# Kernel optimization log

Measured on AMD Instinct MI355X. Metric: run time of the kernel, lower is better.

Reference implementation:

```python
import jax, jax.numpy as jnp
import numpy as np

NUM_HEADS = 8


def setup_inputs() -> dict:
    key = jax.random.key(0)
    k1, k2 = jax.random.split(key)
    B, N, C = 2, 8192, 512
    x = jax.random.normal(k1, (B, N, C), dtype=jnp.float32)
    # torch nn.Linear weight layout: [out_features, in_features]
    W_qkv = jax.random.normal(k2, (3 * C, C), dtype=jnp.float32) * (C ** -0.5)
    return {"x": x, "W_qkv": W_qkv}


def reference(x, W_qkv):
    B, N, C = x.shape
    H = NUM_HEADS
    d = C // H
    scale = d ** -0.5

    # qkv projection (no bias): [B, N, 3C]
    qkv = x @ W_qkv.T
    # [B, N, 3, H, d] -> [3, B, H, N, d]
    qkv = qkv.reshape(B, N, 3, H, d).transpose(2, 0, 3, 1, 4)
    q, k, v = qkv[0], qkv[1], qkv[2]

    # mean-center keys over sequence dim
    k_hat = k - jnp.mean(k, axis=2, keepdims=True)          # [B, H, N, d]

    # KV aggregation: g = k_hat^T @ v  -> [B, H, d, d]
    g = jnp.einsum('bhnd,bhne->bhde', k_hat, v)

    # k_sum over sequence (numerically ~0 since k_hat is centered, kept faithful)
    k_sum = jnp.sum(k_hat, axis=2)                          # [B, H, d]
    q_ksum = jnp.einsum('bhnd,bhd->bhn', q, k_sum)[..., None]  # [B, H, N, 1]

    # denominator: N*scale + q @ k_sum^T
    t_D = N * scale + q_ksum                                # [B, H, N, 1]
    # numerator: scale + q @ g (broadcast of ones*scale over last dim)
    T_N = scale + jnp.einsum('bhnd,bhde->bhne', q, g)       # [B, H, N, d]

    z = T_N / t_D                                           # [B, H, N, d]
    return z
```

## Files before the change

### kernel.cpp

```cpp
#include <hip/hip_runtime.h>

typedef unsigned short u16;
typedef unsigned int u32;
typedef __attribute__((ext_vector_type(8))) short short8;
typedef __attribute__((ext_vector_type(4))) float f32x4;
typedef __attribute__((ext_vector_type(4))) unsigned short ushort4v;
typedef __attribute__((ext_vector_type(4))) float float4v;

__device__ __forceinline__ float bf2f(u16 u) {
    return __uint_as_float(((u32)u) << 16);
}
__device__ __forceinline__ u16 f2bf(float f) {
    u32 u = __float_as_uint(f);
    u += 0x7FFF + ((u >> 16) & 1);
    return (u16)(u >> 16);
}
__device__ __forceinline__ short8 cvt8(float4 a, float4 b) {
    short8 r;
    r[0] = (short)f2bf(a.x); r[1] = (short)f2bf(a.y);
    r[2] = (short)f2bf(a.z); r[3] = (short)f2bf(a.w);
    r[4] = (short)f2bf(b.x); r[5] = (short)f2bf(b.y);
    r[6] = (short)f2bf(b.z); r[7] = (short)f2bf(b.w);
    return r;
}
__device__ __forceinline__ void stage16(const u16* g, u16* l) {
    __builtin_amdgcn_global_load_lds(
        (const __attribute__((address_space(1))) unsigned int*)g,
        (__attribute__((address_space(3))) unsigned int*)l, 16, 0, 0);
}

__global__ __launch_bounds__(256) void cvt_t(const float* __restrict__ x,
                                             u16* __restrict__ xT,
                                             u16* __restrict__ xb,
                                             float* __restrict__ sp2,
                                             const float* __restrict__ W,
                                             u16* __restrict__ wvb,
                                             u16* __restrict__ Ub) {
    __shared__ __align__(16) char smem[36864];
    const int bid = blockIdx.x;
    const int t = threadIdx.x;
    if (bid >= 1280) {
        const int u = bid - 1280;
        const int h = u >> 4, mt = (u >> 2) & 3, ntt = u & 3;
        u16 (*At)[72] = (u16(*)[72])smem;
        u16 (*Bt)[72] = (u16(*)[72])(smem + 18432);
        const int d = t >> 2, cg = (t & 3) * 32;
        const float* wq = W + (size_t)(h * 64 + d) * 512 + mt * 128 + cg;
        const float* wk = W + (size_t)(512 + h * 64 + d) * 512 + ntt * 128 + cg;
#pragma unroll
        for (int j = 0; j < 32; j += 4) {
            float4 a = *(const float4*)(wq + j);
            float4 kk = *(const float4*)(wk + j);
            At[cg + j + 0][d] = f2bf(a.x); At[cg + j + 1][d] = f2bf(a.y);
            At[cg + j + 2][d] = f2bf(a.z); At[cg + j + 3][d] = f2bf(a.w);
            Bt[cg + j + 0][d] = f2bf(kk.x); Bt[cg + j + 1][d] = f2bf(kk.y);
            Bt[cg + j + 2][d] = f2bf(kk.z); Bt[cg + j + 3][d] = f2bf(kk.w);
        }
        __syncthreads();
        const int l = t & 63, wv = t >> 6;
        const int lr = l & 15, lk = (l >> 4) * 8;
        const int wm = (wv >> 1) * 64, wn = (wv & 1) * 64;
        f32x4 zz = {0.f, 0.f, 0.f, 0.f};
        f32x4 acc[4][4];
        for (int i = 0; i < 4; ++i)
            for (int j = 0; j < 4; ++j) acc[i][j] = zz;
#pragma unroll
        for (int k0 = 0; k0 < 64; k0 += 32) {
            short8 af[4], bfr[4];
#pragma unroll
            for (int mi = 0; mi < 4; ++mi)
                af[mi] = *(const short8*)(&At[wm + mi * 16 + lr][k0 + lk]);
#pragma unroll
            for (int ni = 0; ni < 4; ++ni)
                bfr[ni] = *(const short8*)(&Bt[wn + ni * 16 + lr][k0 + lk]);
#pragma unroll
            for (int mi = 0; mi < 4; ++mi)
#pragma unroll
                for (int ni = 0; ni < 4; ++ni)
                    acc[mi][ni] = __builtin_amdgcn_mfma_f32_16x16x32_bf16(
                        af[mi], bfr[ni], acc[mi][ni], 0, 0, 0);
        }
#pragma unroll
        for (int mi = 0; mi < 4; ++mi)
#pragma unroll
            for (int ni = 0; ni < 4; ++ni) {
                int col = ntt * 128 + wn + ni * 16 + lr;
#pragma unroll
                for (int j = 0; j < 4; ++j) {
                    int row = mt * 128 + wm + mi * 16 + (l >> 4) * 4 + j;
                    Ub[((size_t)(h * 512 + row)) * 512 + col] = f2bf(acc[mi][ni][j]);
                }
            }
        return;
    }
    if (bid >= 1024) {
        const int i = (bid - 1024) * 256 + t;
        float4v v = ((const float4v*)(W + 524288))[i];
        ushort4v r;
        r[0] = f2bf(v[0]); r[1] = f2bf(v[1]); r[2] = f2bf(v[2]); r[3] = f2bf(v[3]);
        ((ushort4v*)wvb)[i] = r;
        return;
    }
    u16 (*tile)[136] = (u16(*)[136])smem;
    const int ct = bid & 3, nt = (bid >> 2) & 127, b = bid >> 9;
    const int r = t >> 2, c0 = (t & 3) * 32;
    const float* src = x + ((size_t)(b * 8192 + nt * 64 + r)) * 512 + ct * 128 + c0;
    short8 r8[4];
#pragma unroll
    for (int j = 0; j < 8; j += 2) {
        float4 v0 = *(const float4*)(src + j * 4);
        float4 v1 = *(const float4*)(src + j * 4 + 4);
        r8[j >> 1] = cvt8(v0, v1);
        *(short8*)(&tile[r][c0 + j * 4]) = r8[j >> 1];
    }
    u16* xbrow = xb + ((size_t)(b * 8192 + nt * 64 + r)) * 512 + ct * 128 + c0;
#pragma unroll
    for (int jj = 0; jj < 4; ++jj) *(short8*)(xbrow + jj * 8) = r8[jj];
    __syncthreads();
    const int c = t >> 1, half = t & 1;
    u16 vals[32];
    float psum = 0.f;
#pragma unroll
    for (int i = 0; i < 32; ++i) {
        vals[i] = tile[half * 32 + i][c];
        psum += bf2f(vals[i]);
    }
    u16* dst = xT + ((size_t)(b * 512 + ct * 128 + c)) * 8192 + nt * 64 + half * 32;
#pragma unroll
    for (int j = 0; j < 4; ++j)
        *(int4*)(dst + j * 8) = *(int4*)(&vals[j * 8]);
    psum += __shfl_xor(psum, 1);
    if ((t & 1) == 0)
        sp2[((size_t)(b * 128 + nt)) * 512 + ct * 128 + c] = psum;
}

template <int STRIDE, int KLEN>
__device__ __forceinline__ void gemm_core(const u16* __restrict__ Ag,
                                          const u16* __restrict__ Bg,
                                          u16* As, u16* Bs, int t,
                                          f32x4 acc[4][4]) {
    const int wv = t >> 6, l = t & 63;
    const int lr = l & 15, lk = (l >> 4) * 8;
    const int wm = (wv >> 1) * 64, wn = (wv & 1) * 64;
    const int srow = l >> 2, scol = (l & 3) * 8;

    u16* Ad0 = As + (wv * 32) * 32;
    u16* Ad1 = As + (wv * 32 + 16) * 32;
    u16* Bd0 = Bs + (wv * 32) * 32;
    u16* Bd1 = Bs + (wv * 32 + 16) * 32;
    const u16* As0 = Ag + (size_t)(wv * 32 + srow) * STRIDE + scol;
    const u16* As1 = Ag + (size_t)(wv * 32 + 16 + srow) * STRIDE + scol;
    const u16* Bs0 = Bg + (size_t)(wv * 32 + srow) * STRIDE + scol;
    const u16* Bs1 = Bg + (size_t)(wv * 32 + 16 + srow) * STRIDE + scol;

    for (int k0 = 0; k0 < KLEN; k0 += 32) {
        stage16(As0 + k0, Ad0);
        stage16(As1 + k0, Ad1);
        stage16(Bs0 + k0, Bd0);
        stage16(Bs1 + k0, Bd1);
        __syncthreads();
        short8 af[4], bfr[4];
#pragma unroll
        for (int mi = 0; mi < 4; ++mi)
            af[mi] = *(const short8*)(As + (wm + mi * 16 + lr) * 32 + lk);
#pragma unroll
        for (int ni = 0; ni < 4; ++ni)
            bfr[ni] = *(const short8*)(Bs + (wn + ni * 16 + lr) * 32 + lk);
#pragma unroll
        for (int mi = 0; mi < 4; ++mi)
#pragma unroll
            for (int ni = 0; ni < 4; ++ni)
                acc[mi][ni] = __builtin_amdgcn_mfma_f32_16x16x32_bf16(
                    af[mi], bfr[ni], acc[mi][ni], 0, 0, 0);
        __syncthreads();
    }
}

__global__ __launch_bounds__(256) void syrk(const u16* __restrict__ xT,
                                            u16* __restrict__ Spart,
                                            const float* __restrict__ sp2,
                                            float* __restrict__ ssum) {
    const int bid = blockIdx.x, t = threadIdx.x;
    if (bid >= 512) {
        const int idx = (bid - 512) * 256 + t;
        const int b = idx >> 9, c = idx & 511;
        float a = 0.f;
        for (int j = 0; j < 128; ++j) a += sp2[(size_t)(b * 128 + j) * 512 + c];
        ssum[idx] = a;
        return;
    }
    __shared__ u16 As[128 * 32];
    __shared__ u16 Bs[128 * 32];
    const int nt = bid & 3, mt = (bid >> 2) & 3;
    const int ks = (bid >> 4) & 15, b = bid >> 8;
    const u16* Ag = xT + ((size_t)(b * 512 + mt * 128)) * 8192 + ks * 512;
    const u16* Bg = xT + ((size_t)(b * 512 + nt * 128)) * 8192 + ks * 512;

    f32x4 zz = {0.f, 0.f, 0.f, 0.f};
    f32x4 acc[4][4];
    for (int i = 0; i < 4; ++i)
        for (int j = 0; j < 4; ++j) acc[i][j] = zz;

    gemm_core<8192, 512>(Ag, Bg, As, Bs, t, acc);

    const int l = t & 63, wv = t >> 6;
    const int lr = l & 15;
    const int wm = (wv >> 1) * 64, wn = (wv & 1) * 64;
    u16* out = Spart + ((size_t)(b * 16 + ks)) * 262144;
#pragma unroll
    for (int mi = 0; mi < 4; ++mi)
#pragma unroll
        for (int ni = 0; ni < 4; ++ni) {
            int col = nt * 128 + wn + ni * 16 + lr;
#pragma unroll
            for (int j = 0; j < 4; ++j) {
                int row = mt * 128 + wm + mi * 16 + (l >> 4) * 4 + j;
                out[(size_t)row * 512 + col] = f2bf(acc[mi][ni][j]);
            }
        }
}

__global__ __launch_bounds__(256) void reduceS(const u16* __restrict__ Spart,
                                               const float* __restrict__ s,
                                               u16* __restrict__ Sbf) {
    const int b = blockIdx.x >> 9, m = blockIdx.x & 511;
    const int t = threadIdx.x;
    const float sm = s[b * 512 + m] * (1.0f / 8192.0f);
#pragma unroll
    for (int rep = 0; rep < 2; ++rep) {
        const int n = rep * 256 + t;
        float acc = 0.f;
#pragma unroll
        for (int ks = 0; ks < 16; ++ks)
            acc += bf2f(Spart[((size_t)(b * 16 + ks)) * 262144 + (size_t)m * 512 + n]);
        acc -= sm * s[b * 512 + n];
        Sbf[(size_t)b * 262144 + (size_t)m * 512 + n] = f2bf(acc);
    }
}

__global__ __launch_bounds__(256) void pgemm(const u16* __restrict__ wvb,
                                             const u16* __restrict__ Sbf,
                                             u16* __restrict__ Pb) {
    __shared__ u16 As[128 * 32];
    __shared__ u16 Bs[128 * 32];
    const int t = threadIdx.x;
    const int nt = blockIdx.x & 3, mt = (blockIdx.x >> 2) & 3, b = blockIdx.x >> 4;
    const u16* Ag = wvb + (size_t)(mt * 128) * 512;
    const u16* Bg = Sbf + (size_t)b * 262144 + (size_t)(nt * 128) * 512;

    f32x4 zz = {0.f, 0.f, 0.f, 0.f};
    f32x4 acc[4][4];
    for (int i = 0; i < 4; ++i)
        for (int j = 0; j < 4; ++j) acc[i][j] = zz;

    gemm_core<512, 512>(Ag, Bg, As, Bs, t, acc);

    const int l = t & 63, wv = t >> 6;
    const int lr = l & 15;
    const int wm = (wv >> 1) * 64, wn = (wv & 1) * 64;
    u16* out = Pb + (size_t)b * 262144;
#pragma unroll
    for (int mi = 0; mi < 4; ++mi)
#pragma unroll
        for (int ni = 0; ni < 4; ++ni) {
            int col = nt * 128 + wn + ni * 16 + lr;
#pragma unroll
            for (int j = 0; j < 4; ++j) {
                int row = mt * 128 + wm + mi * 16 + (l >> 4) * 4 + j;
                out[(size_t)row * 512 + col] = f2bf(acc[mi][ni][j]);
            }
        }
}

__global__ __launch_bounds__(256) void wgg(const u16* __restrict__ Ub,
                                           const u16* __restrict__ Pb,
                                           u16* __restrict__ Wgb) {
    __shared__ u16 As[64 * 32];
    __shared__ u16 Bs[128 * 32];
    const int bh = blockIdx.x >> 2, ct = blockIdx.x & 3;
    const int b = bh >> 3, h = bh & 7;
    const int t = threadIdx.x, wv = t >> 6, l = t & 63;
    const int lr = l & 15, lk = (l >> 4) * 8;
    const int wm = (wv >> 1) * 32, wn = (wv & 1) * 64;
    const int srow = l >> 2, scol = (l & 3) * 8;

    const u16* Ag = Pb + (size_t)b * 262144 + (size_t)(h * 64) * 512;
    const u16* Bg = Ub + (size_t)(h * 512 + ct * 128) * 512;
    u16* Ad = As + (wv * 16) * 32;
    u16* Bd0 = Bs + (wv * 32) * 32;
    u16* Bd1 = Bs + (wv * 32 + 16) * 32;
    const u16* As0 = Ag + (size_t)(wv * 16 + srow) * 512 + scol;
    const u16* Bs0 = Bg + (size_t)(wv * 32 + srow) * 512 + scol;
    const u16* Bs1 = Bg + (size_t)(wv * 32 + 16 + srow) * 512 + scol;

    f32x4 zz = {0.f, 0.f, 0.f, 0.f};
    f32x4 acc[2][4];
    for (int i = 0; i < 2; ++i)
        for (int j = 0; j < 4; ++j) acc[i][j] = zz;

    for (int k0 = 0; k0 < 512; k0 += 32) {
        stage16(As0 + k0, Ad);
        stage16(Bs0 + k0, Bd0);
        stage16(Bs1 + k0, Bd1);
        __syncthreads();
        short8 af[2], bfr[4];
#pragma unroll
        for (int mi = 0; mi < 2; ++mi)
            af[mi] = *(const short8*)(As + (wm + mi * 16 + lr) * 32 + lk);
#pragma unroll
        for (int ni = 0; ni < 4; ++ni)
            bfr[ni] = *(const short8*)(Bs + (wn + ni * 16 + lr) * 32 + lk);
#pragma unroll
        for (int mi = 0; mi < 2; ++mi)
#pragma unroll
            for (int ni = 0; ni < 4; ++ni)
                acc[mi][ni] = __builtin_amdgcn_mfma_f32_16x16x32_bf16(
                    af[mi], bfr[ni], acc[mi][ni], 0, 0, 0);
        __syncthreads();
    }
#pragma unroll
    for (int mi = 0; mi < 2; ++mi)
#pragma unroll
        for (int ni = 0; ni < 4; ++ni) {
            int col = ct * 128 + wn + ni * 16 + lr;
#pragma unroll
            for (int j = 0; j < 4; ++j) {
                int row = wm + mi * 16 + (l >> 4) * 4 + j;
                Wgb[((size_t)(b * 512 + h * 64 + row)) * 512 + col] = f2bf(acc[mi][ni][j]);
            }
        }
}

__global__ __launch_bounds__(256) void out_z(const u16* __restrict__ xb,
                                             const u16* __restrict__ Wgb,
                                             float* __restrict__ z) {
    __shared__ u16 As[128 * 32];
    __shared__ u16 Bs[128 * 32];
    const int t = threadIdx.x;
    const int m0 = blockIdx.x * 128;
    const int b = blockIdx.x >> 6;
    const int n0 = blockIdx.y * 128;

    f32x4 zz = {0.f, 0.f, 0.f, 0.f};
    f32x4 acc[4][4];
    for (int i = 0; i < 4; ++i)
        for (int j = 0; j < 4; ++j) acc[i][j] = zz;

    gemm_core<512, 512>(xb + (size_t)m0 * 512,
                        Wgb + (size_t)b * 262144 + (size_t)n0 * 512, As, Bs, t, acc);

    const int l = t & 63, wv = t >> 6;
    const int lr = l & 15;
    const int wm = (wv >> 1) * 64, wn = (wv & 1) * 64;
#pragma unroll
    for (int mi = 0; mi < 4; ++mi)
#pragma unroll
        for (int ni = 0; ni < 4; ++ni) {
            int he = n0 + wn + ni * 16 + lr;
            int h = he >> 6, e = he & 63;
#pragma unroll
            for (int j = 0; j < 4; ++j) {
                int row = m0 + wm + mi * 16 + (l >> 4) * 4 + j;
                int nidx = row & 8191;
                z[((size_t)(b * 8 + h) * 8192 + nidx) * 64 + e] =
                    (acc[mi][ni][j] + 0.125f) * 0.0009765625f;
            }
        }
}

extern "C" void kernel_launch(void* const* d_in, const int* in_sizes, int n_in,
                              void* d_out, int out_size, void* d_ws, size_t ws_size,
                              hipStream_t stream) {
    const float* x = (const float*)d_in[0];
    const float* W = (const float*)d_in[1];
    float* z = (float*)d_out;

    char* ws = (char*)d_ws;
    u16* xT      = (u16*)(ws);
    u16* xb      = (u16*)(ws + 16777216);
    u16* Spart   = (u16*)(ws + 33554432);
    u16* Sbf     = (u16*)(ws + 50331648);
    float* sp2   = (float*)(ws + 51380224);
    float* ssum  = (float*)(ws + 51904512);
    u16* wvb     = (u16*)(ws + 51908608);
    u16* Pb      = (u16*)(ws + 52432896);
    u16* Ub      = (u16*)(ws + 53481472);
    u16* Wgb     = (u16*)(ws + 57675776);

    cvt_t<<<1408, 256, 0, stream>>>(x, xT, xb, sp2, W, wvb, Ub);
    syrk<<<516, 256, 0, stream>>>(xT, Spart, sp2, ssum);
    reduceS<<<1024, 256, 0, stream>>>(Spart, ssum, Sbf);
    pgemm<<<32, 256, 0, stream>>>(wvb, Sbf, Pb);
    wgg<<<64, 256, 0, stream>>>(Ub, Pb, Wgb);
    out_z<<<dim3(128, 4), 256, 0, stream>>>(xb, Wgb, z);
}
```

Measured before the change: 85.34 us.

## Split-K the small pgemm and wgg GEMMs with fp32 partials and reduce kernels

The pgemm and wgg kernels launched only 32 and 64 blocks, which leaves most of the GPU's compute units idle. Each is now split four ways along K, giving 128 and 256 blocks. The fp32 partial results are summed by two new reduce kernels, and reduceS is also changed to load and store two bf16 values per thread. The cost is two extra launches and extra global memory traffic for the fp32 partials.

```diff
diff --git a/kernel.cpp b/kernel.cpp
--- a/kernel.cpp
+++ b/kernel.cpp
@@ -226,39 +226,43 @@
     const int b = blockIdx.x >> 9, m = blockIdx.x & 511;
     const int t = threadIdx.x;
     const float sm = s[b * 512 + m] * (1.0f / 8192.0f);
-#pragma unroll
-    for (int rep = 0; rep < 2; ++rep) {
-        const int n = rep * 256 + t;
-        float acc = 0.f;
-#pragma unroll
-        for (int ks = 0; ks < 16; ++ks)
-            acc += bf2f(Spart[((size_t)(b * 16 + ks)) * 262144 + (size_t)m * 512 + n]);
-        acc -= sm * s[b * 512 + n];
-        Sbf[(size_t)b * 262144 + (size_t)m * 512 + n] = f2bf(acc);
-    }
+    const int n0 = t * 2;
+    float a0 = 0.f, a1 = 0.f;
+#pragma unroll
+    for (int ks = 0; ks < 16; ++ks) {
+        u32 v = *(const u32*)(Spart + ((size_t)(b * 16 + ks)) * 262144 +
+                              (size_t)m * 512 + n0);
+        a0 += bf2f((u16)(v & 0xffff));
+        a1 += bf2f((u16)(v >> 16));
+    }
+    a0 -= sm * s[b * 512 + n0];
+    a1 -= sm * s[b * 512 + n0 + 1];
+    u32 packed = (u32)f2bf(a0) | ((u32)f2bf(a1) << 16);
+    *(u32*)(Sbf + (size_t)b * 262144 + (size_t)m * 512 + n0) = packed;
 }
 
 __global__ __launch_bounds__(256) void pgemm(const u16* __restrict__ wvb,
                                              const u16* __restrict__ Sbf,
-                                             u16* __restrict__ Pb) {
+                                             float* __restrict__ Ppart) {
     __shared__ u16 As[128 * 32];
     __shared__ u16 Bs[128 * 32];
     const int t = threadIdx.x;
-    const int nt = blockIdx.x & 3, mt = (blockIdx.x >> 2) & 3, b = blockIdx.x >> 4;
-    const u16* Ag = wvb + (size_t)(mt * 128) * 512;
-    const u16* Bg = Sbf + (size_t)b * 262144 + (size_t)(nt * 128) * 512;
+    const int nt = blockIdx.x & 3, mt = (blockIdx.x >> 2) & 3;
+    const int ks = (blockIdx.x >> 4) & 3, b = blockIdx.x >> 6;
+    const u16* Ag = wvb + (size_t)(mt * 128) * 512 + ks * 128;
+    const u16* Bg = Sbf + (size_t)b * 262144 + (size_t)(nt * 128) * 512 + ks * 128;
 
     f32x4 zz = {0.f, 0.f, 0.f, 0.f};
     f32x4 acc[4][4];
     for (int i = 0; i < 4; ++i)
         for (int j = 0; j < 4; ++j) acc[i][j] = zz;
 
-    gemm_core<512, 512>(Ag, Bg, As, Bs, t, acc);
+    gemm_core<512, 128>(Ag, Bg, As, Bs, t, acc);
 
     const int l = t & 63, wv = t >> 6;
     const int lr = l & 15;
     const int wm = (wv >> 1) * 64, wn = (wv & 1) * 64;
-    u16* out = Pb + (size_t)b * 262144;
+    float* out = Ppart + ((size_t)(b * 4 + ks)) * 262144;
 #pragma unroll
     for (int mi = 0; mi < 4; ++mi)
 #pragma unroll
@@ -267,25 +271,38 @@
 #pragma unroll
             for (int j = 0; j < 4; ++j) {
                 int row = mt * 128 + wm + mi * 16 + (l >> 4) * 4 + j;
-                out[(size_t)row * 512 + col] = f2bf(acc[mi][ni][j]);
+                out[(size_t)row * 512 + col] = acc[mi][ni][j];
             }
         }
+}
+
+__global__ __launch_bounds__(256) void reduceP(const float* __restrict__ Ppart,
+                                               u16* __restrict__ Pb) {
+    int idx = blockIdx.x * 1024 + threadIdx.x;
+    for (int r = 0; r < 4; ++r, idx += 256) {
+        const int b = idx >> 18, rem = idx & 262143;
+        float acc = 0.f;
+#pragma unroll
+        for (int ks = 0; ks < 4; ++ks)
+            acc += Ppart[((size_t)(b * 4 + ks)) * 262144 + rem];
+        Pb[idx] = f2bf(acc);
+    }
 }
 
 __global__ __launch_bounds__(256) void wgg(const u16* __restrict__ Ub,
                                            const u16* __restrict__ Pb,
-                                           u16* __restrict__ Wgb) {
+                                           float* __restrict__ Wgpart) {
     __shared__ u16 As[64 * 32];
     __shared__ u16 Bs[128 * 32];
-    const int bh = blockIdx.x >> 2, ct = blockIdx.x & 3;
+    const int ks = blockIdx.x & 3, ct = (blockIdx.x >> 2) & 3, bh = blockIdx.x >> 4;
     const int b = bh >> 3, h = bh & 7;
     const int t = threadIdx.x, wv = t >> 6, l = t & 63;
     const int lr = l & 15, lk = (l >> 4) * 8;
     const int wm = (wv >> 1) * 32, wn = (wv & 1) * 64;
     const int srow = l >> 2, scol = (l & 3) * 8;
 
-    const u16* Ag = Pb + (size_t)b * 262144 + (size_t)(h * 64) * 512;
-    const u16* Bg = Ub + (size_t)(h * 512 + ct * 128) * 512;
+    const u16* Ag = Pb + (size_t)b * 262144 + (size_t)(h * 64) * 512 + ks * 128;
+    const u16* Bg = Ub + (size_t)(h * 512 + ct * 128) * 512 + ks * 128;
     u16* Ad = As + (wv * 16) * 32;
     u16* Bd0 = Bs + (wv * 32) * 32;
     u16* Bd1 = Bs + (wv * 32 + 16) * 32;
@@ -298,7 +315,7 @@
     for (int i = 0; i < 2; ++i)
         for (int j = 0; j < 4; ++j) acc[i][j] = zz;
 
-    for (int k0 = 0; k0 < 512; k0 += 32) {
+    for (int k0 = 0; k0 < 128; k0 += 32) {
         stage16(As0 + k0, Ad);
         stage16(Bs0 + k0, Bd0);
         stage16(Bs1 + k0, Bd1);
@@ -326,9 +343,22 @@
 #pragma unroll
             for (int j = 0; j < 4; ++j) {
                 int row = wm + mi * 16 + (l >> 4) * 4 + j;
-                Wgb[((size_t)(b * 512 + h * 64 + row)) * 512 + col] = f2bf(acc[mi][ni][j]);
+                Wgpart[((size_t)(ks * 1024 + b * 512 + h * 64 + row)) * 512 + col] =
+                    acc[mi][ni][j];
             }
         }
+}
+
+__global__ __launch_bounds__(256) void reduceW(const float* __restrict__ Wgpart,
+                                               u16* __restrict__ Wgb) {
+    int idx = blockIdx.x * 1024 + threadIdx.x;
+    for (int r = 0; r < 4; ++r, idx += 256) {
+        float acc = 0.f;
+#pragma unroll
+        for (int ks = 0; ks < 4; ++ks)
+            acc += Wgpart[(size_t)ks * 524288 + idx];
+        Wgb[idx] = f2bf(acc);
+    }
 }
 
 __global__ __launch_bounds__(256) void out_z(const u16* __restrict__ xb,
@@ -376,21 +406,25 @@
     float* z = (float*)d_out;
 
     char* ws = (char*)d_ws;
-    u16* xT      = (u16*)(ws);
-    u16* xb      = (u16*)(ws + 16777216);
-    u16* Spart   = (u16*)(ws + 33554432);
-    u16* Sbf     = (u16*)(ws + 50331648);
-    float* sp2   = (float*)(ws + 51380224);
-    float* ssum  = (float*)(ws + 51904512);
-    u16* wvb     = (u16*)(ws + 51908608);
-    u16* Pb      = (u16*)(ws + 52432896);
-    u16* Ub      = (u16*)(ws + 53481472);
-    u16* Wgb     = (u16*)(ws + 57675776);
+    u16* xT       = (u16*)(ws);
+    u16* xb       = (u16*)(ws + 16777216);
+    u16* Spart    = (u16*)(ws + 33554432);
+    u16* Sbf      = (u16*)(ws + 50331648);
+    float* sp2    = (float*)(ws + 51380224);
+    float* ssum   = (float*)(ws + 51904512);
+    u16* wvb      = (u16*)(ws + 51908608);
+    u16* Pb       = (u16*)(ws + 52432896);
+    u16* Ub       = (u16*)(ws + 53481472);
+    u16* Wgb      = (u16*)(ws + 57675776);
+    float* Ppart  = (float*)(ws + 58724352);
+    float* Wgpart = (float*)(ws + 67112960);
 
     cvt_t<<<1408, 256, 0, stream>>>(x, xT, xb, sp2, W, wvb, Ub);
     syrk<<<516, 256, 0, stream>>>(xT, Spart, sp2, ssum);
     reduceS<<<1024, 256, 0, stream>>>(Spart, ssum, Sbf);
-    pgemm<<<32, 256, 0, stream>>>(wvb, Sbf, Pb);
-    wgg<<<64, 256, 0, stream>>>(Ub, Pb, Wgb);
+    pgemm<<<128, 256, 0, stream>>>(wvb, Sbf, Ppart);
+    reduceP<<<512, 256, 0, stream>>>(Ppart, Pb);
+    wgg<<<256, 256, 0, stream>>>(Ub, Pb, Wgpart);
+    reduceW<<<512, 256, 0, stream>>>(Wgpart, Wgb);
     out_z<<<dim3(128, 4), 256, 0, stream>>>(xb, Wgb, z);
 }
```

New measurement: 81.99 us. 3.9% less time.
